# Performance work log

Measured on AMD Instinct MI355X. Metric: run time of the kernel, lower is better.

## Reference

```python
import jax, jax.numpy as jnp
import numpy as np

B, N, D, H = 256, 164, 1024, 8
NK = 100          # keypoint block size (hardcoded 100 in the module)
DH = D // H       # 128


def setup_inputs() -> dict:
    key = jax.random.key(0)
    ks = jax.random.split(key, 10)
    x = jax.random.normal(ks[0], (B, N, D), jnp.float32)
    xian = jax.random.normal(ks[1], (B, NK, NK), jnp.float32)
    # mask: True = masked. Keep the first NK columns unmasked so the dynamic-MLP
    # block never sees -finfo.max values (matches sane usage; avoids overflow).
    mask_tail = jax.random.bernoulli(ks[2], 0.1, (B, N - NK))
    mask = jnp.concatenate([jnp.zeros((B, NK), bool), mask_tail], axis=1)
    Wqkv = jax.random.normal(ks[3], (D, 3 * D), jnp.float32) * 0.02
    W1 = jax.random.normal(ks[4], (NK, 50), jnp.float32) * 0.1
    b1 = jnp.zeros((50,), jnp.float32)
    W2 = jax.random.normal(ks[5], (50, NK), jnp.float32) * 0.1
    b2 = jnp.zeros((NK,), jnp.float32)
    Wout = jax.random.normal(ks[6], (D, D), jnp.float32) * 0.02
    bout = jnp.zeros((D,), jnp.float32)
    return {"x": x, "mask": mask, "xian": xian, "Wqkv": Wqkv,
            "W1": W1, "b1": b1, "W2": W2, "b2": b2,
            "Wout": Wout, "bout": bout}


def reference(x, mask, xian, Wqkv, W1, b1, W2, b2, Wout, bout):
    scale = D ** -0.5  # scale_with_head=False -> dim**-0.5
    qkv = x @ Wqkv                                   # [B,N,3D]
    q, k, v = jnp.split(qkv, 3, axis=-1)
    def heads(t):
        return t.reshape(B, N, H, DH).transpose(0, 2, 1, 3)  # b h n d
    q, k, v = heads(q), heads(k), heads(v)
    dots = jnp.einsum('bhid,bhjd->bhij', q, k) * scale       # [B,H,N,N]
    mask_value = -jnp.finfo(dots.dtype).max
    dots = jnp.where(mask[:, None, None, :], mask_value, dots)
    # dynamic correction on the keypoint block
    aq = dots[:, :, :NK, :NK]                                # [B,H,100,100]
    lv = jax.nn.relu(jax.nn.relu(jax.nn.relu(aq) @ W1 + b1) @ W2 + b2)
    xin = aq + xian[:, None, :, :] * lv
    dots = dots.at[:, :, :NK, :NK].set(xin)
    attn = jax.nn.softmax(dots, axis=-1)
    out = jnp.einsum('bhij,bhjd->bhid', attn, v)             # [B,H,N,DH]
    out = out.transpose(0, 2, 1, 3).reshape(B, N, D)
    return out @ Wout + bout
```

## Files before the change

kernel.cpp:

```cpp
#include <hip/hip_runtime.h>
#include <hip/hip_bf16.h>
#include <cstdint>
#include <cstddef>

typedef __bf16 bf16;
typedef __attribute__((ext_vector_type(8))) __bf16 bf16x8;
typedef __attribute__((ext_vector_type(2))) __bf16 bf16x2;
typedef __attribute__((ext_vector_type(4))) __bf16 bf16x4;
typedef __attribute__((ext_vector_type(4))) float f32x4;

#define DEVI __device__ __forceinline__

constexpr int Bb = 256, Nn = 164, NKk = 100;
constexpr int Mm = Bb * Nn;
constexpr int JP = 192;

DEVI void gl_lds16(const void* g, void* l) {
  __builtin_amdgcn_global_load_lds(
      (const __attribute__((address_space(1))) void*)g,
      (__attribute__((address_space(3))) void*)l, 16, 0, 0);
}

DEVI int sw16(int row, int kb) { return row * 128 + ((kb ^ (row & 7)) * 8); }
DEVI int sw8(int row, int kb)  { return row * 64 + ((kb ^ (row & 7)) * 8); }

DEVI void barrier_raw() {
  asm volatile("" ::: "memory");
  __builtin_amdgcn_s_barrier();
  asm volatile("" ::: "memory");
}
DEVI void vm0_barrier() {
  asm volatile("s_waitcnt vmcnt(0)" ::: "memory");
  __builtin_amdgcn_s_barrier();
  asm volatile("" ::: "memory");
}

__global__ void k_cvt_bf16(const float* __restrict__ in, bf16* __restrict__ out, int n) {
  int stride = gridDim.x * blockDim.x;
  for (int i = blockIdx.x * blockDim.x + threadIdx.x; i < (n >> 2); i += stride) {
    float4 v = ((const float4*)in)[i];
    bf16x4 o;
    o[0] = (bf16)v.x; o[1] = (bf16)v.y; o[2] = (bf16)v.z; o[3] = (bf16)v.w;
    ((bf16x4*)out)[i] = o;
  }
}

__global__ void k_maskdet(const unsigned char* __restrict__ m, int* __restrict__ mode) {
  __shared__ int sbyte, sodd;
  if (threadIdx.x == 0) { sbyte = 0; sodd = 0; }
  __syncthreads();
  for (int i = threadIdx.x; i < Mm; i += 256)
    if ((i & 3) && m[i]) sbyte = 1;
  __syncthreads();
  if (sbyte == 0) {
    const int* m32 = (const int*)m;
    for (int i = 1 + 2 * (int)threadIdx.x; i < Mm; i += 512)
      if (m32[i] != 0) sodd = 1;
  }
  __syncthreads();
  if (threadIdx.x == 0) *mode = sbyte ? 1 : (sodd ? 0 : 2);
}

__global__ void k_prep_w(const float* __restrict__ W1, const float* __restrict__ W2,
                         bf16* __restrict__ w1t, bf16* __restrict__ w2t) {
  int tid = threadIdx.x;
  int4 z = make_int4(0, 0, 0, 0);
  for (int i = tid; i < 1024; i += 256) ((int4*)w1t)[i] = z;
  for (int i = tid; i < 896;  i += 256) ((int4*)w2t)[i] = z;
  __syncthreads();
  for (int idx = tid; idx < 5000; idx += 256) {
    int k = idx / 50, c = idx % 50;
    w1t[sw16(c, k >> 3) + (k & 7)] = (bf16)W1[idx];
  }
  for (int idx = tid; idx < 5000; idx += 256) {
    int c = idx / 100, jp = idx % 100;
    w2t[sw8(jp, c >> 3) + (c & 7)] = (bf16)W2[idx];
  }
}

__global__ void k_maskbias(const void* __restrict__ maskp, const int* __restrict__ mode,
                           float* __restrict__ mb) {
  int b = blockIdx.x, col = threadIdx.x;
  int mmode = *mode;
  float v;
  if (col < NKk) v = 0.f;
  else if (col < 164) {
    int mi = b * 164 + col;
    long long m = (mmode == 1) ? (long long)((const unsigned char*)maskp)[mi]
                : (mmode == 0) ? (long long)((const int*)maskp)[mi]
                               : ((const long long*)maskp)[mi];
    v = m ? -__FLT_MAX__ : 0.f;
  } else v = -__FLT_MAX__;
  mb[b * 192 + col] = v;
}

__global__ void k_xianT(const float* __restrict__ xian, float* __restrict__ xT) {
  __shared__ float t[32][33];
  int b = blockIdx.y;
  int gt = blockIdx.x & 3, jt = blockIdx.x >> 2;
  int tx = threadIdx.x & 31, ty = threadIdx.x >> 5;
#pragma unroll
  for (int i = 0; i < 4; ++i) {
    int gi = gt * 32 + ty + i * 8, jp = jt * 32 + tx;
    t[ty + i * 8][tx] = (gi < 100 && jp < 100) ? xian[((size_t)b * 100 + gi) * 100 + jp] : 0.f;
  }
  __syncthreads();
#pragma unroll
  for (int i = 0; i < 4; ++i) {
    int jp = jt * 32 + ty + i * 8, gi = gt * 32 + tx;
    if (jp < 100 && gi < 112)
      xT[((size_t)b * 100 + jp) * 112 + gi] = t[tx][ty + i * 8];
  }
}

__global__ void k_transpose_cvt(const float* __restrict__ in, bf16* __restrict__ out,
                                int R, int C) {
  __shared__ float tile[32][33];
  int c0 = blockIdx.x * 32, r0 = blockIdx.y * 32;
  int tx = threadIdx.x & 31, ty = threadIdx.x >> 5;
#pragma unroll
  for (int i = 0; i < 4; ++i) {
    int r = ty + i * 8;
    tile[r][tx] = in[(size_t)(r0 + r) * C + c0 + tx];
  }
  __syncthreads();
#pragma unroll
  for (int i = 0; i < 4; ++i) {
    int rr = ty + i * 8;
    out[(size_t)(c0 + rr) * R + r0 + tx] = (bf16)tile[tx][rr];
  }
}

template <int MODE>
__global__ __launch_bounds__(512, 2) void k_gemm(const bf16* __restrict__ A,
                                                 const bf16* __restrict__ Bt,
                                                 void* __restrict__ Cout,
                                                 const float* __restrict__ bias,
                                                 bf16* __restrict__ vTout) {
  constexpr int K = 1024;
  constexpr int NT = 16;
  __shared__ __align__(16) char smem[131072];

  const int tid = threadIdx.x, lane = tid & 63, w = tid >> 6;
  const int l15 = lane & 15, l4 = lane >> 4;
  const int wm = w >> 2, wn = w & 3;

  const int nbx = (MODE == 0) ? 12 : 4;
  const int lin = blockIdx.x;
  const int cpx = gridDim.x >> 3;
  const int swz = (lin & 7) * cpx + (lin >> 3);
  const int tileM = (swz / nbx) * 256, tileN = (swz % nbx) * 256;

  size_t aoff[4], boff[4]; int loff[4];
#pragma unroll
  for (int li = 0; li < 4; ++li) {
    int idx = li * 512 + tid;
    int row = idx >> 3, sl = idx & 7;
    int kb = sl ^ (row & 7);
    aoff[li] = (size_t)(tileM + row) * K + kb * 8;
    boff[li] = (size_t)(tileN + row) * K + kb * 8;
    loff[li] = idx * 16;
  }

  f32x4 acc[8][4];
#pragma unroll
  for (int mf = 0; mf < 8; ++mf)
#pragma unroll
    for (int nf = 0; nf < 4; ++nf) acc[mf][nf] = f32x4{0.f, 0.f, 0.f, 0.f};

#pragma unroll
  for (int li = 0; li < 4; ++li) {
    gl_lds16(A + aoff[li], smem + loff[li]);
    gl_lds16(Bt + boff[li], smem + 65536 + loff[li]);
  }

  for (int t = 0; t < NT; ++t) {
    const int coff = (t & 1) << 15;
    const char* Ac = smem + coff;
    const char* Bc = smem + 65536 + coff;
    char* An = smem + (coff ^ 32768);
    char* Bn = smem + 65536 + (coff ^ 32768);
    const int kadd = (t + 1) * 64;
    const bool st = (t + 1) < NT;

    vm0_barrier();

    bf16x8 bfr[4][2];
#pragma unroll
    for (int nf = 0; nf < 4; ++nf) {
      int row = wn * 64 + nf * 16 + l15;
#pragma unroll
      for (int kk = 0; kk < 2; ++kk)
        bfr[nf][kk] = *(const bf16x8*)(Bc + row * 128 + (((kk * 4 + l4) ^ (row & 7)) * 16));
    }

#pragma unroll
    for (int ph = 0; ph < 4; ++ph) {
      if (st) {
#pragma unroll
        for (int q = 0; q < 2; ++q) {
          int li = (ph & 1) * 2 + q;
          if (ph < 2) gl_lds16(A + aoff[li] + kadd, An + loff[li]);
          else        gl_lds16(Bt + boff[li] + kadd, Bn + loff[li]);
        }
      }
      bf16x8 af[2][2];
#pragma unroll
      for (int mi = 0; mi < 2; ++mi) {
        int row = wm * 128 + (ph * 2 + mi) * 16 + l15;
#pragma unroll
        for (int kk = 0; kk < 2; ++kk)
          af[mi][kk] = *(const bf16x8*)(Ac + row * 128 + (((kk * 4 + l4) ^ (row & 7)) * 16));
      }
      __builtin_amdgcn_s_setprio(1);
#pragma unroll
      for (int mi = 0; mi < 2; ++mi)
#pragma unroll
        for (int nf = 0; nf < 4; ++nf)
#pragma unroll
          for (int kk = 0; kk < 2; ++kk)
            acc[ph * 2 + mi][nf] = __builtin_amdgcn_mfma_f32_16x16x32_bf16(
                af[mi][kk], bfr[nf][kk], acc[ph * 2 + mi][nf], 0, 0, 0);
      __builtin_amdgcn_s_setprio(0);
      barrier_raw();
    }
  }

  if (MODE == 0 && tileN >= 2048) {
    const int h0 = (tileN - 2048) >> 7;
    bf16* Et = (bf16*)smem;
#pragma unroll
    for (int nh = 0; nh < 2; ++nh) {
      barrier_raw();
      if ((wn >> 1) == nh) {
#pragma unroll
        for (int mf = 0; mf < 8; ++mf)
#pragma unroll
          for (int nf = 0; nf < 4; ++nf) {
            int nr = (wn & 1) * 64 + nf * 16 + l15;
            int mr = wm * 128 + mf * 16 + l4 * 4;
            bf16x4 pv;
#pragma unroll
            for (int j = 0; j < 4; ++j) pv[j] = (bf16)acc[mf][nf][j];
            *(bf16x4*)&Et[nr * 264 + mr] = pv;
          }
      }
      barrier_raw();
#pragma unroll
      for (int r8 = 0; r8 < 8; ++r8) {
        int idx = r8 * 512 + tid;
        int nr = idx >> 5, m8 = (idx & 31) * 8;
        bf16x8 v = *(const bf16x8*)&Et[nr * 264 + m8];
        int m = tileM + m8;
        int b = m / 164, j = m - b * 164;
        if (j + 7 < 164) {
          size_t base = ((size_t)(b * 8 + h0 + nh) * 128 + nr) * JP + j;
          bf16x4 lo, hi;
#pragma unroll
          for (int e = 0; e < 4; ++e) { lo[e] = v[e]; hi[e] = v[e + 4]; }
          *(bf16x4*)&vTout[base] = lo;
          *(bf16x4*)&vTout[base + 4] = hi;
        } else {
#pragma unroll
          for (int e = 0; e < 8; ++e) {
            int me = m + e; int be = me / 164, je = me - be * 164;
            vTout[((size_t)(be * 8 + h0 + nh) * 128 + nr) * JP + je] = v[e];
          }
        }
      }
    }
  } else {
#pragma unroll
    for (int mf = 0; mf < 8; ++mf)
#pragma unroll
      for (int nf = 0; nf < 4; ++nf) {
        int m0 = tileM + wm * 128 + mf * 16 + l4 * 4;
        int n = tileN + wn * 64 + nf * 16 + l15;
        if (MODE == 0) {
#pragma unroll
          for (int j = 0; j < 4; ++j)
            ((bf16*)Cout)[(size_t)(m0 + j) * 3072 + n] = (bf16)acc[mf][nf][j];
        } else {
          float bv = bias[n];
#pragma unroll
          for (int j = 0; j < 4; ++j)
            ((float*)Cout)[(size_t)(m0 + j) * 1024 + n] = acc[mf][nf][j] + bv;
        }
      }
  }
}

__global__ __launch_bounds__(704, 3) void k_attn(
    const bf16* __restrict__ qkv, const bf16* __restrict__ vT,
    const bf16* __restrict__ w1t_g, const bf16* __restrict__ w2t_g,
    const float* __restrict__ maskbias, const float* __restrict__ xianT,
    const float* __restrict__ b1, const float* __restrict__ b2,
    bf16* __restrict__ aout) {
  __shared__ __align__(16) char smem[160448];
  bf16* VTs = (bf16*)smem;
  bf16* Ks  = (bf16*)(smem + 49152);
  bf16* AQs = (bf16*)(smem + 49152);
  bf16* Pw0 = (bf16*)(smem + 94208);
  bf16* W1T = (bf16*)(smem + 128000);
  bf16* H1s = (bf16*)(smem + 128000);
  bf16* W2T = (bf16*)(smem + 144384);
  float* biasL = (float*)(smem + 158720);
  float* b1L = (float*)(smem + 159744);
  float* b2L = (float*)(smem + 160000);

  const int tid = threadIdx.x, lane = tid & 63, w = tid >> 6;
  const int l15 = lane & 15, l4 = lane >> 4;
  const int i0 = blockIdx.x;
  const int bh = (i0 & 7) * 256 + (i0 >> 3);
  const int b = bh >> 3, h = bh & 7;
  const int rq = w * 16;
  const int pr12 = l15 % 12;

  bf16x8 qf[4];
  {
    int qrow = rq + l15; if (qrow > 163) qrow = 163;
    const bf16* qbase = qkv + (size_t)(b * 164 + qrow) * 3072 + h * 128;
#pragma unroll
    for (int kk = 0; kk < 4; ++kk)
      qf[kk] = *(const bf16x8*)(qbase + kk * 32 + l4 * 8);
  }

  for (int c = w; c < 41; c += 11) {
    int blk = c * 64 + lane;
    int r = blk >> 4, sl = blk & 15;
    int kb = sl ^ (r & 7);
    gl_lds16(qkv + (size_t)(b * 164 + r) * 3072 + 1024 + h * 128 + kb * 8, (char*)Ks + c * 1024);
  }
  for (int c = w; c < 48; c += 11) {
    int blk = c * 64 + lane;
    int dh = blk / 24, sl = blk % 24;
    int kb = sl - (dh % 24); if (kb < 0) kb += 24;
    gl_lds16(vT + ((size_t)bh * 128 + dh) * JP + kb * 8, (char*)VTs + c * 1024);
  }
  for (int c = w; c < 16; c += 11)
    gl_lds16(w1t_g + c * 512 + lane * 8, (char*)W1T + c * 1024);
  for (int c = w; c < 14; c += 11)
    gl_lds16(w2t_g + c * 512 + lane * 8, (char*)W2T + c * 1024);
  if (w == 10 && lane < 48)
    gl_lds16(maskbias + b * 192 + lane * 4, (char*)biasL);
  if (tid < 192) {
    int r = 164 + (tid >> 4), sl = tid & 15;
    ((int4*)Ks)[r * 16 + sl] = make_int4(0, 0, 0, 0);
  }
  if (tid < 64) b1L[tid] = (tid < 50) ? b1[tid] : 0.f;
  else if (tid < 176) { int c = tid - 64; b2L[c] = (c < 100) ? b2[c] : 0.f; }
  __syncthreads();

  constexpr float SC = 0.03125f;
  f32x4 s[11];
#pragma unroll
  for (int nt = 0; nt < 11; ++nt) {
    f32x4 acc = f32x4{0.f, 0.f, 0.f, 0.f};
#pragma unroll
    for (int kk = 0; kk < 4; ++kk) {
      bf16x8 kf = *(const bf16x8*)&Ks[sw16(nt * 16 + l15, kk * 4 + l4)];
      acc = __builtin_amdgcn_mfma_f32_16x16x32_bf16(kf, qf[kk], acc, 0, 0, 0);
    }
    f32x4 bv = *(const f32x4*)&biasL[nt * 16 + l4 * 4];
#pragma unroll
    for (int j = 0; j < 4; ++j) acc[j] = acc[j] * SC + bv[j];
    s[nt] = acc;
  }
  __syncthreads();

  if (w < 7) {
    int q = rq + l15;
#pragma unroll
    for (int nt = 0; nt < 8; ++nt) {
#pragma unroll
      for (int pr = 0; pr < 2; ++pr) {
        int k0 = nt * 16 + l4 * 4 + pr * 2;
        float v0 = (q < 100 && k0 < 100)     ? fmaxf(s[nt][pr * 2], 0.f)     : 0.f;
        float v1 = (q < 100 && k0 + 1 < 100) ? fmaxf(s[nt][pr * 2 + 1], 0.f) : 0.f;
        bf16x2 pv; pv[0] = (bf16)v0; pv[1] = (bf16)v1;
        *(bf16x2*)&AQs[sw16(q, k0 >> 3) + (k0 & 7)] = pv;
      }
    }
  }
  __syncthreads();

  f32x4 a1[3];
#pragma unroll
  for (int it = 0; it < 3; ++it) {
    int t = w + it * 11;
    f32x4 acc = f32x4{0.f, 0.f, 0.f, 0.f};
    if (t < 28) {
      int qs = t >> 2, ct = t & 3;
#pragma unroll
      for (int kk = 0; kk < 4; ++kk) {
        bf16x8 wf = *(const bf16x8*)&W1T[sw16(ct * 16 + l15, kk * 4 + l4)];
        bf16x8 af = *(const bf16x8*)&AQs[sw16(qs * 16 + l15, kk * 4 + l4)];
        acc = __builtin_amdgcn_mfma_f32_16x16x32_bf16(wf, af, acc, 0, 0, 0);
      }
    }
    a1[it] = acc;
  }
  __syncthreads();
#pragma unroll
  for (int it = 0; it < 3; ++it) {
    int t = w + it * 11;
    if (t < 28) {
      int qs = t >> 2, ct = t & 3;
      int qrow = qs * 16 + l15;
#pragma unroll
      for (int pr = 0; pr < 2; ++pr) {
        int c0 = ct * 16 + l4 * 4 + pr * 2;
        float v0 = (c0 < 50)     ? fmaxf(a1[it][pr * 2] + b1L[c0], 0.f)         : 0.f;
        float v1 = (c0 + 1 < 50) ? fmaxf(a1[it][pr * 2 + 1] + b1L[c0 + 1], 0.f) : 0.f;
        bf16x2 pv; pv[0] = (bf16)v0; pv[1] = (bf16)v1;
        *(bf16x2*)&H1s[sw8(qrow, c0 >> 3) + (c0 & 7)] = pv;
      }
    }
  }
  __syncthreads();

  if (w < 7) {
    int q = rq + l15;
#pragma unroll
    for (int nt2 = 0; nt2 < 7; ++nt2) {
      f32x4 acc = f32x4{0.f, 0.f, 0.f, 0.f};
#pragma unroll
      for (int kk = 0; kk < 2; ++kk) {
        bf16x8 wf = *(const bf16x8*)&W2T[sw8(nt2 * 16 + l15, kk * 4 + l4)];
        bf16x8 hf = *(const bf16x8*)&H1s[sw8(rq + l15, kk * 4 + l4)];
        acc = __builtin_amdgcn_mfma_f32_16x16x32_bf16(wf, hf, acc, 0, 0, 0);
      }
#pragma unroll
      for (int j = 0; j < 4; ++j) {
        int jp = nt2 * 16 + l4 * 4 + j;
        if (jp < 100 && q < 100) {
          float lv = fmaxf(acc[j] + b2L[jp], 0.f);
          s[nt2][j] += xianT[((size_t)b * 100 + jp) * 112 + q] * lv;
        }
      }
    }
  }

  float mx = -__FLT_MAX__;
#pragma unroll
  for (int nt = 0; nt < 11; ++nt)
#pragma unroll
    for (int j = 0; j < 4; ++j) mx = fmaxf(mx, s[nt][j]);
  mx = fmaxf(mx, __shfl_xor(mx, 16));
  mx = fmaxf(mx, __shfl_xor(mx, 32));
  float sum = 0.f;
#pragma unroll
  for (int nt = 0; nt < 11; ++nt)
#pragma unroll
    for (int j = 0; j < 4; ++j) { float e = __expf(s[nt][j] - mx); s[nt][j] = e; sum += e; }
  sum += __shfl_xor(sum, 16);
  sum += __shfl_xor(sum, 32);
  float rinv = 1.f / sum;

  bf16x2 pp[11][2];
#pragma unroll
  for (int nt = 0; nt < 11; ++nt)
#pragma unroll
    for (int pr = 0; pr < 2; ++pr) {
      bf16x2 pv;
      pv[0] = (bf16)(s[nt][pr * 2] * rinv);
      pv[1] = (bf16)(s[nt][pr * 2 + 1] * rinv);
      pp[nt][pr] = pv;
    }

  bf16* PwB = Pw0 + w * 1536;
  f32x4 o[8];
#pragma unroll
  for (int i = 0; i < 8; ++i) o[i] = f32x4{0.f, 0.f, 0.f, 0.f};
  int vmr[8];
#pragma unroll
  for (int i = 0; i < 8; ++i) vmr[i] = (i * 16 + l15) % 24;
#pragma unroll
  for (int hh = 0; hh < 2; ++hh) {
#pragma unroll
    for (int nn = 0; nn < 6; ++nn) {
      int nt = hh * 6 + nn;
      if (nt < 11) {
        int slot = nn * 2 + (l4 >> 1);
        int rs = slot + pr12; if (rs >= 12) rs -= 12;
#pragma unroll
        for (int pr = 0; pr < 2; ++pr)
          *(bf16x2*)&PwB[l15 * 96 + rs * 8 + (l4 & 1) * 4 + pr * 2] = pp[nt][pr];
      }
    }
#pragma unroll
    for (int kk2 = 0; kk2 < 3; ++kk2) {
      int rs = kk2 * 4 + l4 + pr12; if (rs >= 12) rs -= 12;
      bf16x8 af = *(const bf16x8*)&PwB[l15 * 96 + rs * 8];
#pragma unroll
      for (int i = 0; i < 8; ++i) {
        int sb = 12 * hh + kk2 * 4 + l4 + vmr[i]; if (sb >= 24) sb -= 24;
        bf16x8 bb = *(const bf16x8*)&VTs[(i * 16 + l15) * 192 + sb * 8];
        o[i] = __builtin_amdgcn_mfma_f32_16x16x32_bf16(af, bb, o[i], 0, 0, 0);
      }
    }
  }

#pragma unroll
  for (int i = 0; i < 8; ++i) {
    int dh = i * 16 + l15;
#pragma unroll
    for (int j = 0; j < 4; ++j) {
      int q = rq + l4 * 4 + j;
      if (q < 164)
        aout[(size_t)(b * 164 + q) * 1024 + h * 128 + dh] = (bf16)o[i][j];
    }
  }
}

extern "C" void kernel_launch(void* const* d_in, const int* in_sizes, int n_in,
                              void* d_out, int out_size, void* d_ws, size_t ws_size,
                              hipStream_t stream) {
  const float* x    = (const float*)d_in[0];
  const void* mask  = (const void*)d_in[1];
  const float* xian = (const float*)d_in[2];
  const float* Wqkv = (const float*)d_in[3];
  const float* W1   = (const float*)d_in[4];
  const float* b1   = (const float*)d_in[5];
  const float* W2   = (const float*)d_in[6];
  const float* b2   = (const float*)d_in[7];
  const float* Wout = (const float*)d_in[8];
  const float* bout = (const float*)d_in[9];
  float* out = (float*)d_out;
  char* ws = (char*)d_ws;

  bf16* xb    = (bf16*)(ws);
  bf16* wqkvT = (bf16*)(ws + 85983232ULL);
  bf16* woutT = (bf16*)(ws + 92274688ULL);
  bf16* qkvb  = (bf16*)(ws + 94371840ULL);
  bf16* vTb   = (bf16*)(ws + 352321536ULL);
  bf16* aoutb = (bf16*)(ws + 452984832ULL);
  int*   mmode    = (int*)(ws + 1024);
  bf16*  w1t_g    = (bf16*)(ws + 4096);
  bf16*  w2t_g    = (bf16*)(ws + 20480);
  float* maskbias = (float*)(ws + 36864);
  float* xianTp   = (float*)(ws + 262144);

  k_cvt_bf16<<<2048, 256, 0, stream>>>(x, xb, Mm * 1024);
  k_transpose_cvt<<<dim3(96, 32), 256, 0, stream>>>(Wqkv, wqkvT, 1024, 3072);
  k_transpose_cvt<<<dim3(32, 32), 256, 0, stream>>>(Wout, woutT, 1024, 1024);
  k_gemm<0><<<1968, 512, 0, stream>>>(xb, wqkvT, (void*)qkvb, nullptr, vTb);
  k_maskdet<<<1, 256, 0, stream>>>((const unsigned char*)mask, mmode);
  k_prep_w<<<1, 256, 0, stream>>>(W1, W2, w1t_g, w2t_g);
  k_maskbias<<<256, 192, 0, stream>>>(mask, mmode, maskbias);
  k_xianT<<<dim3(16, 256), 256, 0, stream>>>(xian, xianTp);
  k_attn<<<2048, 704, 0, stream>>>(qkvb, vTb, w1t_g, w2t_g, maskbias, xianTp,
                                   b1, b2, aoutb);
  k_gemm<1><<<656, 512, 0, stream>>>(aoutb, woutT, (void*)out, bout, nullptr);
}
```

Before: 752.1 us.

## Split attention block by query halves and shrink LDS footprint

Each (batch, head) attention block is split into two query-half blocks of 6 waves each, which doubles the grid and shrinks shared memory from about 160KB to 60KB so more blocks can be resident per CU. K, the MLP weights, the mask bias and the biases are now read straight from global memory instead of being staged in LDS. V is staged in two halves that reuse one buffer. The trade-off is redundant K and weight reads from global/L2 and an extra barrier-separated V reload phase. Only the first query-half block, plus wave 0 of the second, runs the keypoint MLP.

After: 983.1 us. +30.7%, slower.

```diff
diff --git a/kernel.cpp b/kernel.cpp
--- a/kernel.cpp
+++ b/kernel.cpp
@@ -70,11 +70,11 @@
   __syncthreads();
   for (int idx = tid; idx < 5000; idx += 256) {
     int k = idx / 50, c = idx % 50;
-    w1t[sw16(c, k >> 3) + (k & 7)] = (bf16)W1[idx];
+    w1t[c * 128 + k] = (bf16)W1[idx];
   }
   for (int idx = tid; idx < 5000; idx += 256) {
     int c = idx / 100, jp = idx % 100;
-    w2t[sw8(jp, c >> 3) + (c & 7)] = (bf16)W2[idx];
+    w2t[jp * 64 + c] = (bf16)W2[idx];
   }
 }
 
@@ -290,31 +290,35 @@
   }
 }
 
-__global__ __launch_bounds__(704, 3) void k_attn(
+__global__ __launch_bounds__(384, 3) void k_attn(
     const bf16* __restrict__ qkv, const bf16* __restrict__ vT,
-    const bf16* __restrict__ w1t_g, const bf16* __restrict__ w2t_g,
+    const bf16* __restrict__ w1t_p, const bf16* __restrict__ w2t_p,
     const float* __restrict__ maskbias, const float* __restrict__ xianT,
     const float* __restrict__ b1, const float* __restrict__ b2,
     bf16* __restrict__ aout) {
-  __shared__ __align__(16) char smem[160448];
-  bf16* VTs = (bf16*)smem;
-  bf16* Ks  = (bf16*)(smem + 49152);
-  bf16* AQs = (bf16*)(smem + 49152);
-  bf16* Pw0 = (bf16*)(smem + 94208);
-  bf16* W1T = (bf16*)(smem + 128000);
-  bf16* H1s = (bf16*)(smem + 128000);
-  bf16* W2T = (bf16*)(smem + 144384);
-  float* biasL = (float*)(smem + 158720);
-  float* b1L = (float*)(smem + 159744);
-  float* b2L = (float*)(smem + 160000);
+  __shared__ __align__(16) char smem[61440];
+  bf16* Vh  = (bf16*)smem;
+  bf16* AQs = (bf16*)(smem + 24576);
+  bf16* Pw0 = (bf16*)(smem + 24576);
+  bf16* H1s = (bf16*)(smem + 49152);
 
   const int tid = threadIdx.x, lane = tid & 63, w = tid >> 6;
   const int l15 = lane & 15, l4 = lane >> 4;
   const int i0 = blockIdx.x;
-  const int bh = (i0 & 7) * 256 + (i0 >> 3);
+  const int bhq = (i0 & 7) * 512 + (i0 >> 3);
+  const int bh = bhq >> 1, qh = bhq & 1;
   const int b = bh >> 3, h = bh & 7;
-  const int rq = w * 16;
+  const int q0 = qh ? 96 : 0;
+  const int rq = q0 + w * 16;
   const int pr12 = l15 % 12;
+
+#pragma unroll
+  for (int c = w; c < 24; c += 6) {
+    int g = c * 64 + lane;
+    int dh = g / 12, t = g % 12;
+    int ks = t - (dh % 12); if (ks < 0) ks += 12;
+    gl_lds16(vT + (size_t)bh * 24576 + dh * 192 + ks * 8, (char*)Vh + c * 1024);
+  }
 
   bf16x8 qf[4];
   {
@@ -325,51 +329,27 @@
       qf[kk] = *(const bf16x8*)(qbase + kk * 32 + l4 * 8);
   }
 
-  for (int c = w; c < 41; c += 11) {
-    int blk = c * 64 + lane;
-    int r = blk >> 4, sl = blk & 15;
-    int kb = sl ^ (r & 7);
-    gl_lds16(qkv + (size_t)(b * 164 + r) * 3072 + 1024 + h * 128 + kb * 8, (char*)Ks + c * 1024);
-  }
-  for (int c = w; c < 48; c += 11) {
-    int blk = c * 64 + lane;
-    int dh = blk / 24, sl = blk % 24;
-    int kb = sl - (dh % 24); if (kb < 0) kb += 24;
-    gl_lds16(vT + ((size_t)bh * 128 + dh) * JP + kb * 8, (char*)VTs + c * 1024);
-  }
-  for (int c = w; c < 16; c += 11)
-    gl_lds16(w1t_g + c * 512 + lane * 8, (char*)W1T + c * 1024);
-  for (int c = w; c < 14; c += 11)
-    gl_lds16(w2t_g + c * 512 + lane * 8, (char*)W2T + c * 1024);
-  if (w == 10 && lane < 48)
-    gl_lds16(maskbias + b * 192 + lane * 4, (char*)biasL);
-  if (tid < 192) {
-    int r = 164 + (tid >> 4), sl = tid & 15;
-    ((int4*)Ks)[r * 16 + sl] = make_int4(0, 0, 0, 0);
-  }
-  if (tid < 64) b1L[tid] = (tid < 50) ? b1[tid] : 0.f;
-  else if (tid < 176) { int c = tid - 64; b2L[c] = (c < 100) ? b2[c] : 0.f; }
-  __syncthreads();
-
   constexpr float SC = 0.03125f;
   f32x4 s[11];
 #pragma unroll
   for (int nt = 0; nt < 11; ++nt) {
+    int krow = nt * 16 + l15; if (krow > 163) krow = 163;
+    const bf16* kbase = qkv + (size_t)(b * 164 + krow) * 3072 + 1024 + h * 128;
     f32x4 acc = f32x4{0.f, 0.f, 0.f, 0.f};
 #pragma unroll
     for (int kk = 0; kk < 4; ++kk) {
-      bf16x8 kf = *(const bf16x8*)&Ks[sw16(nt * 16 + l15, kk * 4 + l4)];
+      bf16x8 kf = *(const bf16x8*)(kbase + kk * 32 + l4 * 8);
       acc = __builtin_amdgcn_mfma_f32_16x16x32_bf16(kf, qf[kk], acc, 0, 0, 0);
     }
-    f32x4 bv = *(const f32x4*)&biasL[nt * 16 + l4 * 4];
+    f32x4 bv = *(const f32x4*)(maskbias + (size_t)b * 192 + nt * 16 + l4 * 4);
 #pragma unroll
     for (int j = 0; j < 4; ++j) acc[j] = acc[j] * SC + bv[j];
     s[nt] = acc;
   }
-  __syncthreads();
-
-  if (w < 7) {
-    int q = rq + l15;
+
+  if (qh == 0 || w == 0) {
+    int lrow = w * 16 + l15;
+    int q = q0 + lrow;
 #pragma unroll
     for (int nt = 0; nt < 8; ++nt) {
 #pragma unroll
@@ -378,63 +358,63 @@
         float v0 = (q < 100 && k0 < 100)     ? fmaxf(s[nt][pr * 2], 0.f)     : 0.f;
         float v1 = (q < 100 && k0 + 1 < 100) ? fmaxf(s[nt][pr * 2 + 1], 0.f) : 0.f;
         bf16x2 pv; pv[0] = (bf16)v0; pv[1] = (bf16)v1;
-        *(bf16x2*)&AQs[sw16(q, k0 >> 3) + (k0 & 7)] = pv;
-      }
-    }
-  }
-  __syncthreads();
-
-  f32x4 a1[3];
-#pragma unroll
-  for (int it = 0; it < 3; ++it) {
-    int t = w + it * 11;
+        *(bf16x2*)&AQs[sw16(lrow, k0 >> 3) + (k0 & 7)] = pv;
+      }
+    }
+  }
+  __syncthreads();
+
+  const int nt1 = (qh == 0) ? 24 : 4;
+  f32x4 a1[4];
+#pragma unroll
+  for (int it = 0; it < 4; ++it) {
+    int t = w + it * 6;
     f32x4 acc = f32x4{0.f, 0.f, 0.f, 0.f};
-    if (t < 28) {
+    if (t < nt1) {
       int qs = t >> 2, ct = t & 3;
 #pragma unroll
       for (int kk = 0; kk < 4; ++kk) {
-        bf16x8 wf = *(const bf16x8*)&W1T[sw16(ct * 16 + l15, kk * 4 + l4)];
+        bf16x8 wf = *(const bf16x8*)(w1t_p + (ct * 16 + l15) * 128 + (kk * 4 + l4) * 8);
         bf16x8 af = *(const bf16x8*)&AQs[sw16(qs * 16 + l15, kk * 4 + l4)];
         acc = __builtin_amdgcn_mfma_f32_16x16x32_bf16(wf, af, acc, 0, 0, 0);
       }
     }
     a1[it] = acc;
   }
-  __syncthreads();
-#pragma unroll
-  for (int it = 0; it < 3; ++it) {
-    int t = w + it * 11;
-    if (t < 28) {
+#pragma unroll
+  for (int it = 0; it < 4; ++it) {
+    int t = w + it * 6;
+    if (t < nt1) {
       int qs = t >> 2, ct = t & 3;
-      int qrow = qs * 16 + l15;
+      int lrow = qs * 16 + l15;
 #pragma unroll
       for (int pr = 0; pr < 2; ++pr) {
         int c0 = ct * 16 + l4 * 4 + pr * 2;
-        float v0 = (c0 < 50)     ? fmaxf(a1[it][pr * 2] + b1L[c0], 0.f)         : 0.f;
-        float v1 = (c0 + 1 < 50) ? fmaxf(a1[it][pr * 2 + 1] + b1L[c0 + 1], 0.f) : 0.f;
+        float v0 = (c0 < 50)     ? fmaxf(a1[it][pr * 2] + b1[c0], 0.f)         : 0.f;
+        float v1 = (c0 + 1 < 50) ? fmaxf(a1[it][pr * 2 + 1] + b1[c0 + 1], 0.f) : 0.f;
         bf16x2 pv; pv[0] = (bf16)v0; pv[1] = (bf16)v1;
-        *(bf16x2*)&H1s[sw8(qrow, c0 >> 3) + (c0 & 7)] = pv;
-      }
-    }
-  }
-  __syncthreads();
-
-  if (w < 7) {
+        *(bf16x2*)&H1s[sw8(lrow, c0 >> 3) + (c0 & 7)] = pv;
+      }
+    }
+  }
+  __syncthreads();
+
+  if (qh == 0 || w == 0) {
     int q = rq + l15;
 #pragma unroll
     for (int nt2 = 0; nt2 < 7; ++nt2) {
       f32x4 acc = f32x4{0.f, 0.f, 0.f, 0.f};
 #pragma unroll
       for (int kk = 0; kk < 2; ++kk) {
-        bf16x8 wf = *(const bf16x8*)&W2T[sw8(nt2 * 16 + l15, kk * 4 + l4)];
-        bf16x8 hf = *(const bf16x8*)&H1s[sw8(rq + l15, kk * 4 + l4)];
+        bf16x8 wf = *(const bf16x8*)(w2t_p + (nt2 * 16 + l15) * 64 + (kk * 4 + l4) * 8);
+        bf16x8 hf = *(const bf16x8*)&H1s[sw8(w * 16 + l15, kk * 4 + l4)];
         acc = __builtin_amdgcn_mfma_f32_16x16x32_bf16(wf, hf, acc, 0, 0, 0);
       }
 #pragma unroll
       for (int j = 0; j < 4; ++j) {
         int jp = nt2 * 16 + l4 * 4 + j;
         if (jp < 100 && q < 100) {
-          float lv = fmaxf(acc[j] + b2L[jp], 0.f);
+          float lv = fmaxf(acc[j] + b2[jp], 0.f);
           s[nt2][j] += xianT[((size_t)b * 100 + jp) * 112 + q] * lv;
         }
       }
@@ -474,30 +454,56 @@
   for (int i = 0; i < 8; ++i) o[i] = f32x4{0.f, 0.f, 0.f, 0.f};
   int vmr[8];
 #pragma unroll
-  for (int i = 0; i < 8; ++i) vmr[i] = (i * 16 + l15) % 24;
-#pragma unroll
-  for (int hh = 0; hh < 2; ++hh) {
-#pragma unroll
-    for (int nn = 0; nn < 6; ++nn) {
-      int nt = hh * 6 + nn;
-      if (nt < 11) {
-        int slot = nn * 2 + (l4 >> 1);
-        int rs = slot + pr12; if (rs >= 12) rs -= 12;
-#pragma unroll
-        for (int pr = 0; pr < 2; ++pr)
-          *(bf16x2*)&PwB[l15 * 96 + rs * 8 + (l4 & 1) * 4 + pr * 2] = pp[nt][pr];
-      }
-    }
-#pragma unroll
-    for (int kk2 = 0; kk2 < 3; ++kk2) {
-      int rs = kk2 * 4 + l4 + pr12; if (rs >= 12) rs -= 12;
-      bf16x8 af = *(const bf16x8*)&PwB[l15 * 96 + rs * 8];
-#pragma unroll
-      for (int i = 0; i < 8; ++i) {
-        int sb = 12 * hh + kk2 * 4 + l4 + vmr[i]; if (sb >= 24) sb -= 24;
-        bf16x8 bb = *(const bf16x8*)&VTs[(i * 16 + l15) * 192 + sb * 8];
-        o[i] = __builtin_amdgcn_mfma_f32_16x16x32_bf16(af, bb, o[i], 0, 0, 0);
-      }
+  for (int i = 0; i < 8; ++i) vmr[i] = (i * 16 + l15) % 12;
+
+#pragma unroll
+  for (int nn = 0; nn < 6; ++nn) {
+    int slot = nn * 2 + (l4 >> 1);
+    int rs = slot + pr12; if (rs >= 12) rs -= 12;
+#pragma unroll
+    for (int pr = 0; pr < 2; ++pr)
+      *(bf16x2*)&PwB[l15 * 96 + rs * 8 + (l4 & 1) * 4 + pr * 2] = pp[nn][pr];
+  }
+#pragma unroll
+  for (int kk2 = 0; kk2 < 3; ++kk2) {
+    int rs = kk2 * 4 + l4 + pr12; if (rs >= 12) rs -= 12;
+    bf16x8 af = *(const bf16x8*)&PwB[l15 * 96 + rs * 8];
+#pragma unroll
+    for (int i = 0; i < 8; ++i) {
+      int sb = kk2 * 4 + l4 + vmr[i]; if (sb >= 12) sb -= 12;
+      bf16x8 bb = *(const bf16x8*)&Vh[(i * 16 + l15) * 96 + sb * 8];
+      o[i] = __builtin_amdgcn_mfma_f32_16x16x32_bf16(af, bb, o[i], 0, 0, 0);
+    }
+  }
+  __syncthreads();
+
+#pragma unroll
+  for (int c = w; c < 24; c += 6) {
+    int g = c * 64 + lane;
+    int dh = g / 12, t = g % 12;
+    int ks = t - (dh % 12); if (ks < 0) ks += 12;
+    gl_lds16(vT + (size_t)bh * 24576 + dh * 192 + 96 + ks * 8, (char*)Vh + c * 1024);
+  }
+#pragma unroll
+  for (int nn = 0; nn < 5; ++nn) {
+    int nt = 6 + nn;
+    int slot = nn * 2 + (l4 >> 1);
+    int rs = slot + pr12; if (rs >= 12) rs -= 12;
+#pragma unroll
+    for (int pr = 0; pr < 2; ++pr)
+      *(bf16x2*)&PwB[l15 * 96 + rs * 8 + (l4 & 1) * 4 + pr * 2] = pp[nt][pr];
+  }
+  __syncthreads();
+
+#pragma unroll
+  for (int kk2 = 0; kk2 < 3; ++kk2) {
+    int rs = kk2 * 4 + l4 + pr12; if (rs >= 12) rs -= 12;
+    bf16x8 af = *(const bf16x8*)&PwB[l15 * 96 + rs * 8];
+#pragma unroll
+    for (int i = 0; i < 8; ++i) {
+      int sb = kk2 * 4 + l4 + vmr[i]; if (sb >= 12) sb -= 12;
+      bf16x8 bb = *(const bf16x8*)&Vh[(i * 16 + l15) * 96 + sb * 8];
+      o[i] = __builtin_amdgcn_mfma_f32_16x16x32_bf16(af, bb, o[i], 0, 0, 0);
     }
   }
 
@@ -549,7 +555,7 @@
   k_prep_w<<<1, 256, 0, stream>>>(W1, W2, w1t_g, w2t_g);
   k_maskbias<<<256, 192, 0, stream>>>(mask, mmode, maskbias);
   k_xianT<<<dim3(16, 256), 256, 0, stream>>>(xian, xianTp);
-  k_attn<<<2048, 704, 0, stream>>>(qkvb, vTb, w1t_g, w2t_g, maskbias, xianTp,
+  k_attn<<<4096, 384, 0, stream>>>(qkvb, vTb, w1t_g, w2t_g, maskbias, xianTp,
                                    b1, b2, aoutb);
   k_gemm<1><<<656, 512, 0, stream>>>(aoutb, woutT, (void*)out, bout, nullptr);
 }
```

## Triple-buffer GEMM K-loop with 32-wide stages and overlap attention V/weight loads

Applied to the files above, without the earlier changes.

The bf16 GEMM main loop moves from a double-buffered 64-wide K stage with four barriers per step to a three-stage ring of 32-wide K stages. It uses a new 64-byte-row swizzle and waits with vmcnt(4), so two stages stay in flight while one is computed, and LDS use drops from 128KB to 96KB. In the attention kernel, the mask-bias, padding and bias setup plus its __syncthreads now come right after the K-tile load. The V-transpose and MLP weight loads are issued afterwards so they can overlap the QK^T MFMAs. The cost is more loop iterations with less MFMA work per barrier, and the compiler may still insert a full vmcnt wait before __syncthreads.

Measured after the change: 765.7 us. About the same (+1.8%).

```diff
diff --git a/kernel.cpp b/kernel.cpp
--- a/kernel.cpp
+++ b/kernel.cpp
@@ -26,11 +26,6 @@
 
 DEVI void barrier_raw() {
   asm volatile("" ::: "memory");
-  __builtin_amdgcn_s_barrier();
-  asm volatile("" ::: "memory");
-}
-DEVI void vm0_barrier() {
-  asm volatile("s_waitcnt vmcnt(0)" ::: "memory");
   __builtin_amdgcn_s_barrier();
   asm volatile("" ::: "memory");
 }
@@ -138,8 +133,8 @@
                                                  const float* __restrict__ bias,
                                                  bf16* __restrict__ vTout) {
   constexpr int K = 1024;
-  constexpr int NT = 16;
-  __shared__ __align__(16) char smem[131072];
+  constexpr int NT = 32;
+  __shared__ __align__(16) char smem[98304];
 
   const int tid = threadIdx.x, lane = tid & 63, w = tid >> 6;
   const int l15 = lane & 15, l4 = lane >> 4;
@@ -151,12 +146,12 @@
   const int swz = (lin & 7) * cpx + (lin >> 3);
   const int tileM = (swz / nbx) * 256, tileN = (swz % nbx) * 256;
 
-  size_t aoff[4], boff[4]; int loff[4];
-#pragma unroll
-  for (int li = 0; li < 4; ++li) {
+  size_t aoff[2], boff[2]; int loff[2];
+#pragma unroll
+  for (int li = 0; li < 2; ++li) {
     int idx = li * 512 + tid;
-    int row = idx >> 3, sl = idx & 7;
-    int kb = sl ^ (row & 7);
+    int row = idx >> 2, g = idx & 3;
+    int kb = g ^ ((row >> 1) & 3);
     aoff[li] = (size_t)(tileM + row) * K + kb * 8;
     boff[li] = (size_t)(tileN + row) * K + kb * 8;
     loff[li] = idx * 16;
@@ -169,61 +164,81 @@
     for (int nf = 0; nf < 4; ++nf) acc[mf][nf] = f32x4{0.f, 0.f, 0.f, 0.f};
 
 #pragma unroll
-  for (int li = 0; li < 4; ++li) {
-    gl_lds16(A + aoff[li], smem + loff[li]);
-    gl_lds16(Bt + boff[li], smem + 65536 + loff[li]);
-  }
-
-  for (int t = 0; t < NT; ++t) {
-    const int coff = (t & 1) << 15;
-    const char* Ac = smem + coff;
-    const char* Bc = smem + 65536 + coff;
-    char* An = smem + (coff ^ 32768);
-    char* Bn = smem + 65536 + (coff ^ 32768);
-    const int kadd = (t + 1) * 64;
-    const bool st = (t + 1) < NT;
-
-    vm0_barrier();
-
-    bf16x8 bfr[4][2];
+  for (int tt = 0; tt < 2; ++tt)
+#pragma unroll
+    for (int li = 0; li < 2; ++li) {
+      gl_lds16(A + aoff[li] + tt * 32, smem + tt * 32768 + loff[li]);
+      gl_lds16(Bt + boff[li] + tt * 32, smem + tt * 32768 + 16384 + loff[li]);
+    }
+
+  int cur = 0;
+  for (int t = 0; t < NT - 1; ++t) {
+    const char* Ac = smem + cur * 32768;
+    const char* Bc = Ac + 16384;
+    asm volatile("s_waitcnt vmcnt(4)" ::: "memory");
+    __builtin_amdgcn_s_barrier();
+    asm volatile("" ::: "memory");
+
+    if (t + 2 < NT) {
+      int nb = cur + 2; if (nb >= 3) nb -= 3;
+      char* Ln = smem + nb * 32768;
+      const int kadd = (t + 2) * 32;
+#pragma unroll
+      for (int li = 0; li < 2; ++li) {
+        gl_lds16(A + aoff[li] + kadd, Ln + loff[li]);
+        gl_lds16(Bt + boff[li] + kadd, Ln + 16384 + loff[li]);
+      }
+    }
+
+    bf16x8 bfr[4];
 #pragma unroll
     for (int nf = 0; nf < 4; ++nf) {
       int row = wn * 64 + nf * 16 + l15;
-#pragma unroll
-      for (int kk = 0; kk < 2; ++kk)
-        bfr[nf][kk] = *(const bf16x8*)(Bc + row * 128 + (((kk * 4 + l4) ^ (row & 7)) * 16));
-    }
-
-#pragma unroll
-    for (int ph = 0; ph < 4; ++ph) {
-      if (st) {
-#pragma unroll
-        for (int q = 0; q < 2; ++q) {
-          int li = (ph & 1) * 2 + q;
-          if (ph < 2) gl_lds16(A + aoff[li] + kadd, An + loff[li]);
-          else        gl_lds16(Bt + boff[li] + kadd, Bn + loff[li]);
-        }
-      }
-      bf16x8 af[2][2];
-#pragma unroll
-      for (int mi = 0; mi < 2; ++mi) {
-        int row = wm * 128 + (ph * 2 + mi) * 16 + l15;
-#pragma unroll
-        for (int kk = 0; kk < 2; ++kk)
-          af[mi][kk] = *(const bf16x8*)(Ac + row * 128 + (((kk * 4 + l4) ^ (row & 7)) * 16));
-      }
-      __builtin_amdgcn_s_setprio(1);
-#pragma unroll
-      for (int mi = 0; mi < 2; ++mi)
-#pragma unroll
-        for (int nf = 0; nf < 4; ++nf)
-#pragma unroll
-          for (int kk = 0; kk < 2; ++kk)
-            acc[ph * 2 + mi][nf] = __builtin_amdgcn_mfma_f32_16x16x32_bf16(
-                af[mi][kk], bfr[nf][kk], acc[ph * 2 + mi][nf], 0, 0, 0);
-      __builtin_amdgcn_s_setprio(0);
-      barrier_raw();
-    }
+      bfr[nf] = *(const bf16x8*)(Bc + row * 64 + ((l4 ^ ((row >> 1) & 3)) * 16));
+    }
+    bf16x8 af[8];
+#pragma unroll
+    for (int mf = 0; mf < 8; ++mf) {
+      int row = wm * 128 + mf * 16 + l15;
+      af[mf] = *(const bf16x8*)(Ac + row * 64 + ((l4 ^ ((row >> 1) & 3)) * 16));
+    }
+    __builtin_amdgcn_s_setprio(1);
+#pragma unroll
+    for (int mf = 0; mf < 8; ++mf)
+#pragma unroll
+      for (int nf = 0; nf < 4; ++nf)
+        acc[mf][nf] = __builtin_amdgcn_mfma_f32_16x16x32_bf16(
+            af[mf], bfr[nf], acc[mf][nf], 0, 0, 0);
+    __builtin_amdgcn_s_setprio(0);
+
+    cur = (cur + 1 == 3) ? 0 : cur + 1;
+  }
+  {
+    const char* Ac = smem + cur * 32768;
+    const char* Bc = Ac + 16384;
+    asm volatile("s_waitcnt vmcnt(0)" ::: "memory");
+    __builtin_amdgcn_s_barrier();
+    asm volatile("" ::: "memory");
+    bf16x8 bfr[4];
+#pragma unroll
+    for (int nf = 0; nf < 4; ++nf) {
+      int row = wn * 64 + nf * 16 + l15;
+      bfr[nf] = *(const bf16x8*)(Bc + row * 64 + ((l4 ^ ((row >> 1) & 3)) * 16));
+    }
+    bf16x8 af[8];
+#pragma unroll
+    for (int mf = 0; mf < 8; ++mf) {
+      int row = wm * 128 + mf * 16 + l15;
+      af[mf] = *(const bf16x8*)(Ac + row * 64 + ((l4 ^ ((row >> 1) & 3)) * 16));
+    }
+    __builtin_amdgcn_s_setprio(1);
+#pragma unroll
+    for (int mf = 0; mf < 8; ++mf)
+#pragma unroll
+      for (int nf = 0; nf < 4; ++nf)
+        acc[mf][nf] = __builtin_amdgcn_mfma_f32_16x16x32_bf16(
+            af[mf], bfr[nf], acc[mf][nf], 0, 0, 0);
+    __builtin_amdgcn_s_setprio(0);
   }
 
   if (MODE == 0 && tileN >= 2048) {
@@ -331,6 +346,16 @@
     int kb = sl ^ (r & 7);
     gl_lds16(qkv + (size_t)(b * 164 + r) * 3072 + 1024 + h * 128 + kb * 8, (char*)Ks + c * 1024);
   }
+  if (w == 10 && lane < 48)
+    gl_lds16(maskbias + b * 192 + lane * 4, (char*)biasL);
+  if (tid < 192) {
+    int r = 164 + (tid >> 4), sl = tid & 15;
+    ((int4*)Ks)[r * 16 + sl] = make_int4(0, 0, 0, 0);
+  }
+  if (tid < 64) b1L[tid] = (tid < 50) ? b1[tid] : 0.f;
+  else if (tid < 176) { int c = tid - 64; b2L[c] = (c < 100) ? b2[c] : 0.f; }
+  __syncthreads();
+
   for (int c = w; c < 48; c += 11) {
     int blk = c * 64 + lane;
     int dh = blk / 24, sl = blk % 24;
@@ -341,15 +366,6 @@
     gl_lds16(w1t_g + c * 512 + lane * 8, (char*)W1T + c * 1024);
   for (int c = w; c < 14; c += 11)
     gl_lds16(w2t_g + c * 512 + lane * 8, (char*)W2T + c * 1024);
-  if (w == 10 && lane < 48)
-    gl_lds16(maskbias + b * 192 + lane * 4, (char*)biasL);
-  if (tid < 192) {
-    int r = 164 + (tid >> 4), sl = tid & 15;
-    ((int4*)Ks)[r * 16 + sl] = make_int4(0, 0, 0, 0);
-  }
-  if (tid < 64) b1L[tid] = (tid < 50) ? b1[tid] : 0.f;
-  else if (tid < 176) { int c = tid - 64; b2L[c] = (c < 100) ? b2[c] : 0.f; }
-  __syncthreads();
 
   constexpr float SC = 0.03125f;
   f32x4 s[11];
```
